# Kernel tuning notes

Measured on AMD Instinct MI355X. Metric: run time of the kernel, lower is better.

Reference implementation:

```python
import jax, jax.numpy as jnp
import numpy as np

EPS = 1e-05
N_CLUSTERS = 4


def setup_inputs() -> dict:
    key = jax.random.key(0)
    k1, k2, k3, k4, k5, k6 = jax.random.split(key, 6)
    B, C, H, W = 64, 64, 112, 112
    return {
        "x": jax.random.normal(k1, (B, C, H, W), dtype=jnp.float32),
        "running_mean": jax.random.normal(k2, (C,), dtype=jnp.float32),
        "running_var": jax.random.uniform(k3, (C,), dtype=jnp.float32),
        "weight": jax.random.normal(k4, (C,), dtype=jnp.float32),
        "bias": jax.random.normal(k5, (C,), dtype=jnp.float32),
        "labels": jax.random.randint(k6, (B,), 0, N_CLUSTERS, dtype=jnp.int32),
    }


def reference(x, running_mean, running_var, weight, bias, labels):
    B, C, H, W = x.shape
    hw = H * W
    # per-sample partial sums over spatial dims -> [B, C]
    s = jnp.sum(x, axis=(2, 3))
    ss = jnp.sum(x * x, axis=(2, 3))
    # per-cluster reductions over the batch (gather-reduce) -> [G, C]
    S = jax.ops.segment_sum(s, labels, num_segments=N_CLUSTERS)
    SS = jax.ops.segment_sum(ss, labels, num_segments=N_CLUSTERS)
    cnt = jax.ops.segment_sum(jnp.ones((B,), x.dtype), labels, num_segments=N_CLUSTERS)
    N = cnt[:, None] * hw  # elements per (cluster, channel)
    mean_g = S / jnp.maximum(N, 1.0)
    # unbiased variance (ddof=1), matching torch.var_mean(unbiased=True)
    var_g = (SS - N * mean_g * mean_g) / jnp.maximum(N - 1.0, 1.0)
    # blended stats: 0.2 * cluster + 0.8 * running (BN source) stats; scatter back per sample
    mu = 0.2 * mean_g[labels] + 0.8 * running_mean[None, :]      # [B, C]
    var = 0.2 * var_g[labels] + 0.8 * running_var[None, :]       # [B, C]
    x_n = (x - mu[:, :, None, None]) * jax.lax.rsqrt(var + EPS)[:, :, None, None]
    return x_n * weight[None, :, None, None] + bias[None, :, None, None]
```

## Files before the change

kernel.cpp:

```cpp
#include <hip/hip_runtime.h>

#define HW    12544
#define HW4   3136
#define NCH   64
#define NB    64
#define NG    4
#define EPSF  1e-5f


__global__ void cn_init(const int* __restrict__ labels, float* __restrict__ ws) {
    int t = threadIdx.x;
    if (t < 512) ws[t] = 0.0f;
    if (t < NG) {
        int cnt = 0;
        for (int b = 0; b < NB; ++b) cnt += (labels[b] == t) ? 1 : 0;
        ws[512 + t] = (float)cnt;
    }
}

__global__ __launch_bounds__(256) void cn_stats(const float* __restrict__ x,
                                                const int* __restrict__ labels,
                                                float* __restrict__ ws) {
    int p = blockIdx.x;
    int b = p >> 6;
    int c = p & 63;
    const float4* xp = (const float4*)(x + (size_t)p * HW);
    float s = 0.0f, ss = 0.0f;
    for (int i = threadIdx.x; i < HW4; i += 256) {
        float4 v = xp[i];
        s  += v.x + v.y + v.z + v.w;
        ss += v.x * v.x + v.y * v.y + v.z * v.z + v.w * v.w;
    }
    #pragma unroll
    for (int off = 32; off > 0; off >>= 1) {
        s  += __shfl_down(s, off, 64);
        ss += __shfl_down(ss, off, 64);
    }
    __shared__ float sh_s[4], sh_ss[4];
    int lane = threadIdx.x & 63;
    int wave = threadIdx.x >> 6;
    if (lane == 0) { sh_s[wave] = s; sh_ss[wave] = ss; }
    __syncthreads();
    if (threadIdx.x == 0) {
        float ts  = sh_s[0]  + sh_s[1]  + sh_s[2]  + sh_s[3];
        float tss = sh_ss[0] + sh_ss[1] + sh_ss[2] + sh_ss[3];
        int g = labels[b];
        atomicAdd(&ws[g * NCH + c], ts);
        atomicAdd(&ws[256 + g * NCH + c], tss);
    }
}

__global__ __launch_bounds__(256) void cn_norm(const float* __restrict__ x,
                                               const int* __restrict__ labels,
                                               const float* __restrict__ rmean,
                                               const float* __restrict__ rvar,
                                               const float* __restrict__ wgt,
                                               const float* __restrict__ bia,
                                               const float* __restrict__ ws,
                                               float* __restrict__ out) {
    int p = blockIdx.x;
    int b = p >> 6;
    int c = p & 63;
    int g = labels[b];
    float cntf = ws[512 + g];
    float N    = cntf * (float)HW;
    float S    = ws[g * NCH + c];
    float SS   = ws[256 + g * NCH + c];
    float mean = S / fmaxf(N, 1.0f);
    float var  = (SS - N * mean * mean) / fmaxf(N - 1.0f, 1.0f);
    float mu   = 0.2f * mean + 0.8f * rmean[c];
    float vb   = 0.2f * var  + 0.8f * rvar[c];
    float scale = rsqrtf(vb + EPSF) * wgt[c];
    float shift = bia[c] - mu * scale;
    const float4* xp = (const float4*)(x + (size_t)p * HW);
    float4*       op = (float4*)(out + (size_t)p * HW);
    for (int i = threadIdx.x; i < HW4; i += 256) {
        float4 v = xp[i];
        float4 o;
        o.x = v.x * scale + shift;
        o.y = v.y * scale + shift;
        o.z = v.z * scale + shift;
        o.w = v.w * scale + shift;
        op[i] = o;
    }
}

extern "C" void kernel_launch(void* const* d_in, const int* in_sizes, int n_in,
                              void* d_out, int out_size, void* d_ws, size_t ws_size,
                              hipStream_t stream) {
    const float* x      = (const float*)d_in[0];
    const float* rmean  = (const float*)d_in[1];
    const float* rvar   = (const float*)d_in[2];
    const float* wgt    = (const float*)d_in[3];
    const float* bia    = (const float*)d_in[4];
    const int*   labels = (const int*)d_in[5];
    float* out = (float*)d_out;
    float* ws  = (float*)d_ws;

    const int planes = NB * NCH;

    cn_init<<<1, 512, 0, stream>>>(labels, ws);
    cn_stats<<<planes, 256, 0, stream>>>(x, labels, ws);
    cn_norm<<<planes, 256, 0, stream>>>(x, labels, rmean, rvar, wgt, bia, ws, out);
}
```

Measured before the change: 117.7 us.

## Replace atomic cluster accumulation with per-plane stats and in-block segment reduction

The stats kernel now writes one sum and sum-of-squares per (batch, channel) plane instead of atomically adding into per-cluster slots. The normalize kernel reduces those partials per cluster inside each block with a wavefront shuffle and counts cluster members at the same time. This removes the separate init launch and the atomic contention. The output stores also become nontemporal. In exchange, every normalize block redundantly reads 128 partials and runs a small reduction before streaming its plane.

```diff
diff --git a/kernel.cpp b/kernel.cpp
--- a/kernel.cpp
+++ b/kernel.cpp
@@ -4,30 +4,18 @@
 #define HW4   3136
 #define NCH   64
 #define NB    64
-#define NG    4
 #define EPSF  1e-5f
 
+typedef float fvec4 __attribute__((ext_vector_type(4)));
 
-__global__ void cn_init(const int* __restrict__ labels, float* __restrict__ ws) {
-    int t = threadIdx.x;
-    if (t < 512) ws[t] = 0.0f;
-    if (t < NG) {
-        int cnt = 0;
-        for (int b = 0; b < NB; ++b) cnt += (labels[b] == t) ? 1 : 0;
-        ws[512 + t] = (float)cnt;
-    }
-}
 
 __global__ __launch_bounds__(256) void cn_stats(const float* __restrict__ x,
-                                                const int* __restrict__ labels,
                                                 float* __restrict__ ws) {
     int p = blockIdx.x;
-    int b = p >> 6;
-    int c = p & 63;
-    const float4* xp = (const float4*)(x + (size_t)p * HW);
+    const fvec4* xp = (const fvec4*)(x + (size_t)p * HW);
     float s = 0.0f, ss = 0.0f;
     for (int i = threadIdx.x; i < HW4; i += 256) {
-        float4 v = xp[i];
+        fvec4 v = xp[i];
         s  += v.x + v.y + v.z + v.w;
         ss += v.x * v.x + v.y * v.y + v.z * v.z + v.w * v.w;
     }
@@ -36,17 +24,14 @@
         s  += __shfl_down(s, off, 64);
         ss += __shfl_down(ss, off, 64);
     }
-    __shared__ float sh_s[4], sh_ss[4];
+    __shared__ float sh[8];
     int lane = threadIdx.x & 63;
     int wave = threadIdx.x >> 6;
-    if (lane == 0) { sh_s[wave] = s; sh_ss[wave] = ss; }
+    if (lane == 0) { sh[wave] = s; sh[4 + wave] = ss; }
     __syncthreads();
     if (threadIdx.x == 0) {
-        float ts  = sh_s[0]  + sh_s[1]  + sh_s[2]  + sh_s[3];
-        float tss = sh_ss[0] + sh_ss[1] + sh_ss[2] + sh_ss[3];
-        int g = labels[b];
-        atomicAdd(&ws[g * NCH + c], ts);
-        atomicAdd(&ws[256 + g * NCH + c], tss);
+        ws[p]        = sh[0] + sh[1] + sh[2] + sh[3];
+        ws[4096 + p] = sh[4] + sh[5] + sh[6] + sh[7];
     }
 }
 
@@ -61,27 +46,45 @@
     int p = blockIdx.x;
     int b = p >> 6;
     int c = p & 63;
-    int g = labels[b];
-    float cntf = ws[512 + g];
-    float N    = cntf * (float)HW;
-    float S    = ws[g * NCH + c];
-    float SS   = ws[256 + g * NCH + c];
-    float mean = S / fmaxf(N, 1.0f);
-    float var  = (SS - N * mean * mean) / fmaxf(N - 1.0f, 1.0f);
-    float mu   = 0.2f * mean + 0.8f * rmean[c];
-    float vb   = 0.2f * var  + 0.8f * rvar[c];
-    float scale = rsqrtf(vb + EPSF) * wgt[c];
-    float shift = bia[c] - mu * scale;
-    const float4* xp = (const float4*)(x + (size_t)p * HW);
-    float4*       op = (float4*)(out + (size_t)p * HW);
+    __shared__ float sh_scale, sh_shift;
+    if (threadIdx.x < 64) {
+        int t = threadIdx.x;
+        int g  = labels[b];
+        int lb = labels[t];
+        bool m = (lb == g);
+        float s   = m ? ws[t * NCH + c]        : 0.0f;
+        float ss  = m ? ws[4096 + t * NCH + c] : 0.0f;
+        float cnt = m ? 1.0f : 0.0f;
+        #pragma unroll
+        for (int off = 32; off > 0; off >>= 1) {
+            s   += __shfl_down(s,   off, 64);
+            ss  += __shfl_down(ss,  off, 64);
+            cnt += __shfl_down(cnt, off, 64);
+        }
+        if (t == 0) {
+            float N    = cnt * (float)HW;
+            float mean = s / fmaxf(N, 1.0f);
+            float var  = (ss - N * mean * mean) / fmaxf(N - 1.0f, 1.0f);
+            float mu   = 0.2f * mean + 0.8f * rmean[c];
+            float vb   = 0.2f * var  + 0.8f * rvar[c];
+            float scale = rsqrtf(vb + EPSF) * wgt[c];
+            sh_scale = scale;
+            sh_shift = bia[c] - mu * scale;
+        }
+    }
+    __syncthreads();
+    float scale = sh_scale;
+    float shift = sh_shift;
+    const fvec4* xp = (const fvec4*)(x + (size_t)p * HW);
+    fvec4*       op = (fvec4*)(out + (size_t)p * HW);
     for (int i = threadIdx.x; i < HW4; i += 256) {
-        float4 v = xp[i];
-        float4 o;
+        fvec4 v = xp[i];
+        fvec4 o;
         o.x = v.x * scale + shift;
         o.y = v.y * scale + shift;
         o.z = v.z * scale + shift;
         o.w = v.w * scale + shift;
-        op[i] = o;
+        __builtin_nontemporal_store(o, &op[i]);
     }
 }
 
@@ -99,7 +102,6 @@
 
     const int planes = NB * NCH;
 
-    cn_init<<<1, 512, 0, stream>>>(labels, ws);
-    cn_stats<<<planes, 256, 0, stream>>>(x, labels, ws);
+    cn_stats<<<planes, 256, 0, stream>>>(x, ws);
     cn_norm<<<planes, 256, 0, stream>>>(x, labels, rmean, rvar, wgt, bia, ws, out);
 }
```

New measurement: 96.71 us. -17.8%, faster.
